# Kernel tuning notes

Measured on AMD Instinct MI355X. Metric: run time of the kernel, lower is better.

Reference implementation:

```python
import jax, jax.numpy as jnp
import numpy as np

B, LV, D = 8, 4096, 256   # batch, temporal length, channels
N = 2048                   # total ROIs across the batch
P = 32                     # output_size (number of output bins)
G = int(np.ceil(LV / P))   # static max adaptive sampling grid (sampling_ratio=-1)


def setup_inputs() -> dict:
    key = jax.random.key(0)
    k1, k2, k3 = jax.random.split(key, 3)
    feat = jax.random.normal(k1, (B, LV, D), dtype=jnp.float32)
    # boxes: (start, end) along the lv axis, sorted so start <= end, in [0, LV)
    boxes = jnp.sort(
        jax.random.uniform(k2, (N, 2), dtype=jnp.float32, minval=0.0, maxval=float(LV)),
        axis=1,
    )
    batch_idx = jax.random.randint(k3, (N,), 0, B, dtype=jnp.int32)
    return {"feat": feat, "boxes": boxes, "batch_idx": batch_idx}


def _roi_align_1d(feat, boxes, batch_idx):
    # Faithful 1D specialization of torchvision roi_align with boxes
    # (0, y1, 1, y2), output_size=(P, 1), aligned=True, spatial_scale=1,
    # sampling_ratio=-1. The width axis contributes a single sample at x=0
    # with weight 1, so only the y (lv) axis math remains.
    feat_flat = feat.reshape(B * LV, D)
    y1, y2 = boxes[:, 0], boxes[:, 1]
    roi_h = y2 - y1                       # aligned=True: no max(., 1) clamp
    start = y1 - 0.5                      # aligned offset
    bin_h = roi_h / P                     # [N]
    grid_h = jnp.ceil(bin_h).astype(jnp.int32)          # adaptive samples per bin
    count = jnp.maximum(grid_h, 1).astype(feat.dtype)   # avg denominator
    sub = bin_h / jnp.maximum(grid_h, 1)                # spacing inside a bin [N]
    # bin start positions: [N, P]
    bin_off = start[:, None] + jnp.arange(P, dtype=feat.dtype)[None, :] * bin_h[:, None]
    base = batch_idx.astype(jnp.int32) * LV             # [N] row offset into feat_flat

    def bilinear(y):  # y: [N, P] -> [N, P, D]
        valid = (y >= -1.0) & (y <= float(LV))
        yc = jnp.maximum(y, 0.0)
        y_lo = jnp.floor(yc).astype(jnp.int32)
        hi_case = y_lo >= LV - 1
        y_lo = jnp.where(hi_case, LV - 1, y_lo)
        y_hi = jnp.where(hi_case, LV - 1, y_lo + 1)
        yc = jnp.where(hi_case, y_lo.astype(y.dtype), yc)
        ly = yc - y_lo.astype(y.dtype)
        v = (1.0 - ly)[..., None] * feat_flat[base[:, None] + y_lo] \
            + ly[..., None] * feat_flat[base[:, None] + y_hi]
        return jnp.where(valid[..., None], v, 0.0)

    def step(acc, g):
        y = bin_off + (g.astype(feat.dtype) + 0.5) * sub[:, None]   # [N, P]
        m = (g < grid_h)[:, None, None]                              # sample active?
        return acc + jnp.where(m, bilinear(y), 0.0), None

    acc0 = jnp.zeros((N, P, D), dtype=feat.dtype)
    acc, _ = jax.lax.scan(step, acc0, jnp.arange(G, dtype=jnp.int32))
    return acc / count[:, None, None]   # [N, P, D] (torch output after transpose(1,2))


def reference(feat, boxes, batch_idx):
    return _roi_align_1d(feat, boxes, batch_idx)
```

## Files before the change

### kernel.cpp

```cpp
#include <hip/hip_runtime.h>

#define B_    8
#define LV_   4096
#define D_    256
#define N_    2048
#define P_    32
#define WROWS_ 64
#define NWIN_  (B_ * (LV_ / WROWS_))
#define NBINS_ (N_ * P_)
#define CPB_   16

typedef float v4f __attribute__((ext_vector_type(4)));

__device__ __forceinline__ float lane_bcast_f(float v, int l) {
    return __int_as_float(__builtin_amdgcn_readlane(__float_as_int(v), l));
}

__device__ __forceinline__ int bin_r_first(const float* __restrict__ boxes, int n, int p) {
    const float y1 = boxes[2 * n], y2 = boxes[2 * n + 1];
    const float bin_h = (y2 - y1) * (1.0f / (float)P_);
    const int gh = (int)ceilf(bin_h);
    if (gh < 1) return 0;
    const float sub  = bin_h / (float)gh;
    const float boff = (y1 - 0.5f) + (float)p * bin_h;
    const float a    = fmaf(0.5f, sub, boff);
    int r = (int)floorf(a);
    if (r < 0) r = 0;
    if (r > LV_ - 1) r = LV_ - 1;
    return r;
}

__global__ __launch_bounds__(1024) void build_binlist_kernel(
    const float* __restrict__ boxes, const int* __restrict__ batch_idx,
    int* __restrict__ binlist)
{
    __shared__ int cnt[NWIN_], cur[NWIN_];
    const int tid = threadIdx.x;
    for (int i = tid; i < NWIN_; i += 1024) cnt[i] = 0;
    __syncthreads();
    for (int idx = tid; idx < NBINS_; idx += 1024) {
        const int n = idx >> 5, p = idx & 31;
        const int key = (batch_idx[n] << 6) | (bin_r_first(boxes, n, p) >> 6);
        atomicAdd(&cnt[key], 1);
    }
    __syncthreads();
    if (tid == 0) { int s = 0; for (int k = 0; k < NWIN_; ++k) { cur[k] = s; s += cnt[k]; } }
    __syncthreads();
    for (int idx = tid; idx < NBINS_; idx += 1024) {
        const int n = idx >> 5, p = idx & 31;
        const int key = (batch_idx[n] << 6) | (bin_r_first(boxes, n, p) >> 6);
        binlist[atomicAdd(&cur[key], 1)] = idx;
    }
}

__global__ __launch_bounds__(256) void build_order_kernel(
    const int* __restrict__ batch_idx, int* __restrict__ order)
{
    __shared__ int cnt[B_], cur[B_];
    const int tid = threadIdx.x;
    if (tid < B_) cnt[tid] = 0;
    __syncthreads();
    for (int n = tid; n < N_; n += 256) atomicAdd(&cnt[batch_idx[n]], 1);
    __syncthreads();
    if (tid == 0) { int s = 0; for (int b = 0; b < B_; ++b) { cur[b] = s; s += cnt[b]; } }
    __syncthreads();
    for (int n = tid; n < N_; n += 256)
        order[atomicAdd(&cur[batch_idx[n]], 1)] = n;
}

__global__ __launch_bounds__(256) void roi_rows_kernel(
    const float* __restrict__ feat, const float* __restrict__ boxes,
    const int* __restrict__ batch_idx, const int* __restrict__ order,
    float* __restrict__ out)
{
    const int nwg = (N_ * P_) / 4;
    const int cpx = nwg >> 3;
    const int bid = blockIdx.x;
    const int swz = (bid & 7) * cpx + (bid >> 3);
    const int slot = (swz << 2) + (threadIdx.x >> 6);
    const int n    = __builtin_amdgcn_readfirstlane(order[slot >> 5]);
    const int p    = slot & (P_ - 1);
    const int lane = threadIdx.x & 63;
    const int bi   = __builtin_amdgcn_readfirstlane(batch_idx[n]);
    const float y1 = boxes[2 * n], y2 = boxes[2 * n + 1];
    const float bin_h = (y2 - y1) * (1.0f / (float)P_);
    const int gh = (int)ceilf(bin_h);
    const v4f* prow = (const v4f*)feat + (long)bi * (LV_ * (D_ / 4));
    v4f acc0 = {0.f,0.f,0.f,0.f}, acc1 = {0.f,0.f,0.f,0.f};
    if (gh >= 1) {
        const float cntf = (float)gh, sub = bin_h / cntf, inv_sub = 1.0f / sub;
        const float halfsub = 0.5f * sub;
        const float boff = (y1 - 0.5f) + (float)p * bin_h;
        const float a = fmaf(0.5f, sub, boff), ylast = fmaf(cntf - 0.5f, sub, boff);
        int r_first = (int)floorf(a);
        if (r_first < 0) r_first = 0; if (r_first > LV_-1) r_first = LV_-1;
        int r_last = (int)floorf(ylast) + 1;
        if (r_last > LV_-1) r_last = LV_-1; if (r_last < r_first) r_last = r_first;
        const int r0 = __builtin_amdgcn_readfirstlane(r_first);
        const int rl = __builtin_amdgcn_readfirstlane(r_last);
        const float lanef = (float)lane;
        for (int base = r0; base <= rl; base += 64) {
            int kmax = rl - base; if (kmax > 63) kmax = 63;
            const int r = base + lane;
            const float d0 = ((float)base + lanef) - a;
            const float dm = d0 - 1.0f, dp = d0 + 1.0f;
            const float nm = fminf(fmaxf(ceilf(dm * inv_sub), 0.0f), cntf);
            const float n0 = fminf(fmaxf(ceilf(d0 * inv_sub), 0.0f), cntf);
            const float np = fminf(fmaxf(ceilf(dp * inv_sub), 0.0f), cntf);
            float Pm = fmaf(nm, dm, -halfsub * fmaf(nm, nm, -nm));
            float P0 = fmaf(n0, d0, -halfsub * fmaf(n0, n0, -n0));
            float Pp = fmaf(np, dp, -halfsub * fmaf(np, np, -np));
            if (r == 0)       Pm = P0;
            if (r == LV_ - 1) Pp = P0 + cntf;
            const float Wl = (Pm + Pp) - 2.0f * P0;
            const v4f* pS = prow + (long)base * (D_ / 4);
            int k = 0;
            for (; k + 4 <= kmax + 1; k += 4) {
                v4f v0 = pS[lane], v1 = pS[lane+64], v2 = pS[lane+128], v3 = pS[lane+192];
                acc0 += v0 * lane_bcast_f(Wl, k);   acc1 += v1 * lane_bcast_f(Wl, k+1);
                acc0 += v2 * lane_bcast_f(Wl, k+2); acc1 += v3 * lane_bcast_f(Wl, k+3);
                pS += 4 * (D_ / 4);
            }
            for (; k <= kmax; ++k) { v4f v = pS[lane]; acc0 += v * lane_bcast_f(Wl, k); pS += (D_ / 4); }
        }
    }
    const float inv_c = 1.0f / (float)(gh > 1 ? gh : 1);
    v4f res = (acc0 + acc1) * inv_c;
    v4f* op = (v4f*)out + ((long)n * P_ + p) * (D_ / 4) + lane;
    __builtin_nontemporal_store(res, op);
}

__global__ __launch_bounds__(512) void roi_win_kernel(
    const float* __restrict__ feat, const float* __restrict__ boxes,
    const int* __restrict__ batch_idx, const int* __restrict__ binlist,
    float* __restrict__ out)
{
    __shared__ v4f tile[WROWS_ * 64];
    const int nblk = NBINS_ / CPB_;
    const int bid  = blockIdx.x;
    const int blk  = (bid & 7) * (nblk >> 3) + (bid >> 3);
    const int tid  = threadIdx.x;
    const int lane = tid & 63;
    const int wv   = tid >> 6;

    const int idx0 = binlist[blk * CPB_];
    const int wb   = __builtin_amdgcn_readfirstlane(batch_idx[idx0 >> 5]);
    const int wlo  = __builtin_amdgcn_readfirstlane(
                         (bin_r_first(boxes, idx0 >> 5, idx0 & 31) >> 6) << 6);

    {
        const v4f* src = (const v4f*)feat + ((long)wb * LV_ + wlo) * (D_ / 4) + lane;
        const int r0 = wv * 8;
        v4f t0 = src[(r0+0)*64], t1 = src[(r0+1)*64], t2 = src[(r0+2)*64], t3 = src[(r0+3)*64];
        v4f t4 = src[(r0+4)*64], t5 = src[(r0+5)*64], t6 = src[(r0+6)*64], t7 = src[(r0+7)*64];
        v4f* dst = tile + r0 * 64 + lane;
        dst[0]   = t0; dst[64]  = t1; dst[128] = t2; dst[192] = t3;
        dst[256] = t4; dst[320] = t5; dst[384] = t6; dst[448] = t7;
    }
    __syncthreads();

    for (int i = wv; i < CPB_; i += 8) {
        const int idx = __builtin_amdgcn_readfirstlane(binlist[blk * CPB_ + i]);
        const int n = idx >> 5, p = idx & 31;
        const int bi = __builtin_amdgcn_readfirstlane(batch_idx[n]);

        const float y1 = boxes[2 * n], y2 = boxes[2 * n + 1];
        const float bin_h = (y2 - y1) * (1.0f / (float)P_);
        const int gh = (int)ceilf(bin_h);

        const v4f* prow = (const v4f*)feat + (long)bi * (LV_ * (D_ / 4));
        v4f acc0 = {0.f,0.f,0.f,0.f}, acc1 = {0.f,0.f,0.f,0.f};

        if (gh >= 1) {
            const float cntf = (float)gh, sub = bin_h / cntf, inv_sub = 1.0f / sub;
            const float halfsub = 0.5f * sub;
            const float boff = (y1 - 0.5f) + (float)p * bin_h;
            const float a = fmaf(0.5f, sub, boff), ylast = fmaf(cntf - 0.5f, sub, boff);

            int r_first = (int)floorf(a);
            if (r_first < 0) r_first = 0; if (r_first > LV_-1) r_first = LV_-1;
            int r_last = (int)floorf(ylast) + 1;
            if (r_last > LV_-1) r_last = LV_-1; if (r_last < r_first) r_last = r_first;
            const int r0 = __builtin_amdgcn_readfirstlane(r_first);
            const int rl = __builtin_amdgcn_readfirstlane(r_last);
            const float lanef = (float)lane;

            for (int gbase = r0; gbase <= rl; gbase += 64) {
                int kmax = rl - gbase; if (kmax > 63) kmax = 63;

                const int   r  = gbase + lane;
                const float d0 = ((float)gbase + lanef) - a;
                const float dm = d0 - 1.0f, dp = d0 + 1.0f;
                const float nm = fminf(fmaxf(ceilf(dm * inv_sub), 0.0f), cntf);
                const float n0 = fminf(fmaxf(ceilf(d0 * inv_sub), 0.0f), cntf);
                const float np = fminf(fmaxf(ceilf(dp * inv_sub), 0.0f), cntf);
                float Pm = fmaf(nm, dm, -halfsub * fmaf(nm, nm, -nm));
                float P0 = fmaf(n0, d0, -halfsub * fmaf(n0, n0, -n0));
                float Pp = fmaf(np, dp, -halfsub * fmaf(np, np, -np));
                if (r == 0)       Pm = P0;
                if (r == LV_ - 1) Pp = P0 + cntf;
                const float Wl = (Pm + Pp) - 2.0f * P0;

                const int t = kmax + 1;
                int lo, hi;
                if (bi == wb) {
                    lo = wlo - gbase;          lo = lo < 0 ? 0 : (lo > t ? t : lo);
                    hi = wlo + WROWS_ - gbase; hi = hi < lo ? lo : (hi > t ? t : hi);
                } else { lo = t; hi = t; }

#define GSEG(KS, KE) do {                                                        \
    int k = (KS);                                                                \
    const v4f* pS = prow + (long)(gbase + k) * (D_ / 4);                         \
    for (; k + 4 <= (KE); k += 4) {                                              \
        v4f v0 = pS[lane], v1 = pS[lane+64], v2 = pS[lane+128], v3 = pS[lane+192];\
        acc0 += v0 * lane_bcast_f(Wl, k);   acc1 += v1 * lane_bcast_f(Wl, k+1);  \
        acc0 += v2 * lane_bcast_f(Wl, k+2); acc1 += v3 * lane_bcast_f(Wl, k+3);  \
        pS += 4 * (D_ / 4); }                                                    \
    for (; k < (KE); ++k) { v4f v = pS[lane]; acc0 += v * lane_bcast_f(Wl, k); pS += (D_ / 4); } \
} while (0)

                GSEG(0, lo);
                {
                    int k = lo;
                    const v4f* tp = tile + (gbase + lo - wlo) * 64 + lane;
                    for (; k + 4 <= hi; k += 4) {
                        v4f t0 = tp[0], t1 = tp[64], t2 = tp[128], t3 = tp[192];
                        acc0 += t0 * lane_bcast_f(Wl, k);   acc1 += t1 * lane_bcast_f(Wl, k+1);
                        acc0 += t2 * lane_bcast_f(Wl, k+2); acc1 += t3 * lane_bcast_f(Wl, k+3);
                        tp += 256;
                    }
                    for (; k < hi; ++k) { acc0 += tp[0] * lane_bcast_f(Wl, k); tp += 64; }
                }
                GSEG(hi, t);
#undef GSEG
            }
        }

        const float inv_c = 1.0f / (float)(gh > 1 ? gh : 1);
        v4f res = (acc0 + acc1) * inv_c;
        v4f* op = (v4f*)out + ((long)n * P_ + p) * (D_ / 4) + lane;
        __builtin_nontemporal_store(res, op);
    }
}

extern "C" void kernel_launch(void* const* d_in, const int* in_sizes, int n_in,
                              void* d_out, int out_size, void* d_ws, size_t ws_size,
                              hipStream_t stream) {
    const float* feat      = (const float*)d_in[0];
    const float* boxes     = (const float*)d_in[1];
    const int*   batch_idx = (const int*)d_in[2];
    float*       out       = (float*)d_out;

    if (ws_size >= (size_t)NBINS_ * sizeof(int)) {
        int* binlist = (int*)d_ws;
        build_binlist_kernel<<<1, 1024, 0, stream>>>(boxes, batch_idx, binlist);
        roi_win_kernel<<<NBINS_ / CPB_, 512, 0, stream>>>(feat, boxes, batch_idx, binlist, out);
    } else {
        int* order = (int*)d_ws;
        build_order_kernel<<<1, 256, 0, stream>>>(batch_idx, order);
        roi_rows_kernel<<<(N_ * P_) / 4, 256, 0, stream>>>(feat, boxes, batch_idx, order, out);
    }
}
```

Measured before the change: 233.0 us.

## Parallelize bin bucketing into count/scan/scatter kernels and load tiles via LDS DMA

Replaces the single-block bin-list builder with a multi-block count kernel using global atomics, a one-block prefix scan, and a multi-block scatter kernel, so the bucketing runs across many CUs. It also doubles the bins processed per window block and stages the feature tile with global_load_lds direct-to-LDS loads when the builtin exists. The trade-offs are extra launches plus a memset, contended global atomics, and a nondeterministic bin order within each window. The window tile may no longer cover all bins in a block now that each block handles more of them.

```diff
diff --git a/kernel.cpp b/kernel.cpp
--- a/kernel.cpp
+++ b/kernel.cpp
@@ -8,7 +8,7 @@
 #define WROWS_ 64
 #define NWIN_  (B_ * (LV_ / WROWS_))
 #define NBINS_ (N_ * P_)
-#define CPB_   16
+#define CPB_   32
 
 typedef float v4f __attribute__((ext_vector_type(4)));
 
@@ -30,27 +30,41 @@
     return r;
 }
 
-__global__ __launch_bounds__(1024) void build_binlist_kernel(
+__device__ __forceinline__ int bin_key(const float* __restrict__ boxes,
+                                       const int* __restrict__ batch_idx, int idx) {
+    const int n = idx >> 5, p = idx & 31;
+    return (batch_idx[n] << 6) | (bin_r_first(boxes, n, p) >> 6);
+}
+
+__global__ __launch_bounds__(256) void count_bins_kernel(
     const float* __restrict__ boxes, const int* __restrict__ batch_idx,
-    int* __restrict__ binlist)
-{
-    __shared__ int cnt[NWIN_], cur[NWIN_];
-    const int tid = threadIdx.x;
-    for (int i = tid; i < NWIN_; i += 1024) cnt[i] = 0;
-    __syncthreads();
-    for (int idx = tid; idx < NBINS_; idx += 1024) {
-        const int n = idx >> 5, p = idx & 31;
-        const int key = (batch_idx[n] << 6) | (bin_r_first(boxes, n, p) >> 6);
-        atomicAdd(&cnt[key], 1);
-    }
-    __syncthreads();
-    if (tid == 0) { int s = 0; for (int k = 0; k < NWIN_; ++k) { cur[k] = s; s += cnt[k]; } }
-    __syncthreads();
-    for (int idx = tid; idx < NBINS_; idx += 1024) {
-        const int n = idx >> 5, p = idx & 31;
-        const int key = (batch_idx[n] << 6) | (bin_r_first(boxes, n, p) >> 6);
-        binlist[atomicAdd(&cur[key], 1)] = idx;
-    }
+    int* __restrict__ cnt)
+{
+    const int idx = blockIdx.x * 256 + threadIdx.x;
+    atomicAdd(&cnt[bin_key(boxes, batch_idx, idx)], 1);
+}
+
+__global__ __launch_bounds__(NWIN_) void scan_kernel(int* __restrict__ cnt)
+{
+    __shared__ int s[NWIN_];
+    const int t = threadIdx.x;
+    s[t] = cnt[t];
+    __syncthreads();
+    for (int off = 1; off < NWIN_; off <<= 1) {
+        const int v = (t >= off) ? s[t - off] : 0;
+        __syncthreads();
+        s[t] += v;
+        __syncthreads();
+    }
+    cnt[t] = (t == 0) ? 0 : s[t - 1];
+}
+
+__global__ __launch_bounds__(256) void scatter_bins_kernel(
+    const float* __restrict__ boxes, const int* __restrict__ batch_idx,
+    int* __restrict__ cnt, int* __restrict__ binlist)
+{
+    const int idx = blockIdx.x * 256 + threadIdx.x;
+    binlist[atomicAdd(&cnt[bin_key(boxes, batch_idx, idx)], 1)] = idx;
 }
 
 __global__ __launch_bounds__(256) void build_order_kernel(
@@ -149,13 +163,25 @@
                          (bin_r_first(boxes, idx0 >> 5, idx0 & 31) >> 6) << 6);
 
     {
-        const v4f* src = (const v4f*)feat + ((long)wb * LV_ + wlo) * (D_ / 4) + lane;
         const int r0 = wv * 8;
-        v4f t0 = src[(r0+0)*64], t1 = src[(r0+1)*64], t2 = src[(r0+2)*64], t3 = src[(r0+3)*64];
-        v4f t4 = src[(r0+4)*64], t5 = src[(r0+5)*64], t6 = src[(r0+6)*64], t7 = src[(r0+7)*64];
-        v4f* dst = tile + r0 * 64 + lane;
+        const float* srow = feat + ((long)wb * LV_ + wlo + r0) * D_ + lane * 4;
+        v4f* lrow = tile + r0 * 64;
+#if __has_builtin(__builtin_amdgcn_global_load_lds)
+        #pragma unroll
+        for (int j = 0; j < 8; ++j) {
+            __builtin_amdgcn_global_load_lds(
+                (const __attribute__((address_space(1))) void*)(srow + j * D_),
+                (__attribute__((address_space(3))) void*)(lrow + j * 64),
+                16, 0, 0);
+        }
+#else
+        const v4f* src = (const v4f*)feat + ((long)wb * LV_ + wlo + r0) * (D_ / 4) + lane;
+        v4f t0 = src[0],   t1 = src[64],  t2 = src[128], t3 = src[192];
+        v4f t4 = src[256], t5 = src[320], t6 = src[384], t7 = src[448];
+        v4f* dst = lrow + lane;
         dst[0]   = t0; dst[64]  = t1; dst[128] = t2; dst[192] = t3;
         dst[256] = t4; dst[320] = t5; dst[384] = t6; dst[448] = t7;
+#endif
     }
     __syncthreads();
 
@@ -251,9 +277,13 @@
     const int*   batch_idx = (const int*)d_in[2];
     float*       out       = (float*)d_out;
 
-    if (ws_size >= (size_t)NBINS_ * sizeof(int)) {
+    if (ws_size >= (size_t)(NBINS_ + NWIN_) * sizeof(int)) {
         int* binlist = (int*)d_ws;
-        build_binlist_kernel<<<1, 1024, 0, stream>>>(boxes, batch_idx, binlist);
+        int* cnt     = binlist + NBINS_;
+        hipMemsetAsync(cnt, 0, NWIN_ * sizeof(int), stream);
+        count_bins_kernel<<<NBINS_ / 256, 256, 0, stream>>>(boxes, batch_idx, cnt);
+        scan_kernel<<<1, NWIN_, 0, stream>>>(cnt);
+        scatter_bins_kernel<<<NBINS_ / 256, 256, 0, stream>>>(boxes, batch_idx, cnt, binlist);
         roi_win_kernel<<<NBINS_ / CPB_, 512, 0, stream>>>(feat, boxes, batch_idx, binlist, out);
     } else {
         int* order = (int*)d_ws;
```

Result: faster. 212.5 us (-8.8%).
